# Kernel optimization log

Measured on AMD Instinct MI355X. Metric: run time of the kernel, lower is better.

Reference implementation:

```python
import jax, jax.numpy as jnp
import numpy as np

TEMPERATURE = 0.05
EPS = 1e-8  # torch.cosine_similarity eps


def setup_inputs() -> dict:
    key = jax.random.key(0)
    k1, k2 = jax.random.split(key)
    N, D = 8192, 256
    text_embeddings = jax.random.normal(k1, (N, D), dtype=jnp.float32)
    text_pos_embeddings = jax.random.normal(k2, (N, D), dtype=jnp.float32)
    return {"text_embeddings": text_embeddings, "text_pos_embeddings": text_pos_embeddings}


def reference(text_embeddings, text_pos_embeddings):
    # cosine similarity via normalize + single GEMM (same math as broadcasted
    # torch.cosine_similarity, which clamps norms at eps)
    a_norm = jnp.maximum(jnp.linalg.norm(text_embeddings, axis=-1, keepdims=True), EPS)
    b_norm = jnp.maximum(jnp.linalg.norm(text_pos_embeddings, axis=-1, keepdims=True), EPS)
    a = text_embeddings / a_norm  # [N, D]
    b = text_pos_embeddings / b_norm  # [N, D]
    sim = jnp.einsum("nd,md->nm", a, b) / TEMPERATURE  # [N, N]
    # cross-entropy with labels = arange(N): mean over rows of -log_softmax diag
    logp = jax.nn.log_softmax(sim, axis=-1)
    loss = -jnp.mean(jnp.diagonal(logp))
    return loss
```

## Files before the change

kernel.cpp:

```cpp
#include <hip/hip_runtime.h>
#include <math.h>

#define DIM 256

typedef float f32x4 __attribute__((ext_vector_type(4)));
typedef int   i32x8 __attribute__((ext_vector_type(8)));

__constant__ const float kTempInvLog2e = 20.0f * 1.4426950408889634f;
#define LN2 0.6931471805599453f
#define EPS_NORM 1e-8f
#define SCALE_ONE 0x7F7F7F7Fu

static __device__ inline unsigned f2fp8x4(float4 v, float s) {
    int r = 0;
    r = __builtin_amdgcn_cvt_pk_fp8_f32(v.x * s, v.y * s, r, false);
    r = __builtin_amdgcn_cvt_pk_fp8_f32(v.z * s, v.w * s, r, true);
    return (unsigned)r;
}

static __device__ inline i32x8 ld_frag32(const void* p0, const void* p1) {
    uint4 a = *(const uint4*)p0;
    uint4 b = *(const uint4*)p1;
    i32x8 v;
    v[0] = a.x; v[1] = a.y; v[2] = a.z; v[3] = a.w;
    v[4] = b.x; v[5] = b.y; v[6] = b.z; v[7] = b.w;
    return v;
}

__global__ __launch_bounds__(256) void normpack_kernel(
    const float* __restrict__ A, const float* __restrict__ B,
    unsigned char* __restrict__ Apk, unsigned char* __restrict__ Bpk,
    float* __restrict__ diag, float* __restrict__ rowsum, int n)
{
    __shared__ uint4 lA[256];
    __shared__ uint4 lB[256];
    const int t = threadIdx.x;
    const int rl = t >> 4;
    const int c16 = t & 15;
    const int r = blockIdx.x * 16 + rl;

    const float4* pa = (const float4*)(A + (size_t)r * DIM + c16 * 16);
    const float4* pb = (const float4*)(B + (size_t)r * DIM + c16 * 16);
    float4 a0 = pa[0], a1 = pa[1], a2 = pa[2], a3 = pa[3];
    float4 b0 = pb[0], b1 = pb[1], b2 = pb[2], b3 = pb[3];

    float ssa = a0.x*a0.x + a0.y*a0.y + a0.z*a0.z + a0.w*a0.w
              + a1.x*a1.x + a1.y*a1.y + a1.z*a1.z + a1.w*a1.w
              + a2.x*a2.x + a2.y*a2.y + a2.z*a2.z + a2.w*a2.w
              + a3.x*a3.x + a3.y*a3.y + a3.z*a3.z + a3.w*a3.w;
    float ssb = b0.x*b0.x + b0.y*b0.y + b0.z*b0.z + b0.w*b0.w
              + b1.x*b1.x + b1.y*b1.y + b1.z*b1.z + b1.w*b1.w
              + b2.x*b2.x + b2.y*b2.y + b2.z*b2.z + b2.w*b2.w
              + b3.x*b3.x + b3.y*b3.y + b3.z*b3.z + b3.w*b3.w;
    float dd  = a0.x*b0.x + a0.y*b0.y + a0.z*b0.z + a0.w*b0.w
              + a1.x*b1.x + a1.y*b1.y + a1.z*b1.z + a1.w*b1.w
              + a2.x*b2.x + a2.y*b2.y + a2.z*b2.z + a2.w*b2.w
              + a3.x*b3.x + a3.y*b3.y + a3.z*b3.z + a3.w*b3.w;
#pragma unroll
    for (int m = 1; m < 16; m <<= 1) {
        ssa += __shfl_xor(ssa, m, 64);
        ssb += __shfl_xor(ssb, m, 64);
        dd  += __shfl_xor(dd, m, 64);
    }
    float na = fmaxf(sqrtf(ssa), EPS_NORM);
    float nb = fmaxf(sqrtf(ssb), EPS_NORM);
    float sa = kTempInvLog2e / na;
    float sb = 1.0f / nb;
    if (c16 == 0) {
        diag[r] = dd / (na * nb) * kTempInvLog2e;
        rowsum[r] = 0.0f;
    }

    const int u = ((c16 >> 3) << 7) + ((c16 & 1) << 6) + rl + ((c16 & 7) >> 1) * 16;
    uint4 ga, gb;
    ga.x = f2fp8x4(a0, sa); ga.y = f2fp8x4(a1, sa);
    ga.z = f2fp8x4(a2, sa); ga.w = f2fp8x4(a3, sa);
    gb.x = f2fp8x4(b0, sb); gb.y = f2fp8x4(b1, sb);
    gb.z = f2fp8x4(b2, sb); gb.w = f2fp8x4(b3, sb);
    lA[u] = ga; lB[u] = gb;
    __syncthreads();

    ((uint4*)Apk)[(size_t)blockIdx.x * 256 + t] = lA[t];
    ((uint4*)Bpk)[(size_t)blockIdx.x * 256 + t] = lB[t];
}

static __device__ inline void async_copy16(const void* g, void* l) {
    __builtin_amdgcn_global_load_lds(
        (const __attribute__((address_space(1))) unsigned int*)g,
        (__attribute__((address_space(3))) unsigned int*)l, 16, 0, 0);
}

__global__ __launch_bounds__(256, 2) void gemm_lse_kernel(
    const unsigned char* __restrict__ Apk, const unsigned char* __restrict__ Bpk,
    float* __restrict__ rowsum, int n)
{
    __shared__ char ldsbuf[24576];
    const int lane = threadIdx.x & 63;
    const int w = threadIdx.x >> 6;
    const int c = lane & 15;
    const int q = lane >> 4;

    const int i = blockIdx.x;
    const int split = ((i & 7) << 1) | ((i >> 3) & 1);
    const int rowblk = i >> 4;
    const int rowbase = rowblk * 256 + w * 64;

    i32x8 afrag[4][2];
#pragma unroll
    for (int m = 0; m < 4; ++m) {
        const int AT = rowblk * 16 + w * 4 + m;
#pragma unroll
        for (int kc = 0; kc < 2; ++kc) {
            const char* base = (const char*)Apk + ((size_t)AT * 2 + kc) * 2048 + lane * 16;
            afrag[m][kc] = ld_frag32(base, base + 1024);
        }
    }

    float sums[16];
#pragma unroll
    for (int s = 0; s < 16; ++s) sums[s] = 0.0f;

    const char* bbase = (const char*)Bpk + (size_t)split * 32 * 4096;
    const int NITER = 16;

#pragma unroll
    for (int p = 0; p < 2; ++p) {
        const char* src = bbase + (size_t)p * 8192 + w * 2048 + (size_t)lane * 16;
        char* dst = ldsbuf + p * 8192 + w * 2048;
        async_copy16(src, dst);
        async_copy16(src + 1024, dst + 1024);
    }
    asm volatile("s_waitcnt vmcnt(2)" ::: "memory");
    __builtin_amdgcn_s_barrier();

#pragma unroll
    for (int it = 0; it < NITER; ++it) {
#pragma unroll
        for (int m = 0; m < 4; ++m)
#pragma unroll
            for (int kc = 0; kc < 2; ++kc)
                asm volatile("" : "+v"(afrag[m][kc]));

        const int cur = it % 3;
        const char* lb = ldsbuf + cur * 8192 + (size_t)lane * 16;

        i32x8 bfrag[2][2];
#pragma unroll
        for (int nc = 0; nc < 2; ++nc)
#pragma unroll
            for (int kc = 0; kc < 2; ++kc) {
                const char* p = lb + nc * 4096 + kc * 2048;
                bfrag[nc][kc] = ld_frag32(p, p + 1024);
            }

        if (it + 2 < NITER) {
            const int nb = (it + 2) % 3;
            const char* src = bbase + (size_t)(it + 2) * 8192 + w * 2048 + (size_t)lane * 16;
            char* dst = ldsbuf + nb * 8192 + w * 2048;
            async_copy16(src, dst);
            async_copy16(src + 1024, dst + 1024);
        }

        f32x4 acc[4][2];
#pragma unroll
        for (int m = 0; m < 4; ++m)
#pragma unroll
            for (int nc = 0; nc < 2; ++nc)
                acc[m][nc] = (f32x4){0.f, 0.f, 0.f, 0.f};

#pragma unroll
        for (int nc = 0; nc < 2; ++nc)
#pragma unroll
            for (int kc = 0; kc < 2; ++kc)
#pragma unroll
                for (int m = 0; m < 4; ++m)
                    acc[m][nc] = __builtin_amdgcn_mfma_scale_f32_16x16x128_f8f6f4(
                        afrag[m][kc], bfrag[nc][kc], acc[m][nc],
                        0, 0,
                        0, SCALE_ONE,
                        0, SCALE_ONE);

#pragma unroll
        for (int m = 0; m < 4; ++m)
#pragma unroll
            for (int nc = 0; nc < 2; ++nc)
#pragma unroll
                for (int r = 0; r < 4; ++r)
                    sums[m * 4 + r] += __builtin_amdgcn_exp2f(acc[m][nc][r]);

        if (it + 2 < NITER) {
            asm volatile("s_waitcnt vmcnt(2)" ::: "memory");
            __builtin_amdgcn_s_barrier();
        } else if (it + 1 < NITER) {
            asm volatile("s_waitcnt vmcnt(0)" ::: "memory");
            __builtin_amdgcn_s_barrier();
        }
    }

#pragma unroll
    for (int s = 0; s < 16; ++s) {
        float v = sums[s];
        v += __shfl_xor(v, 1, 64);
        v += __shfl_xor(v, 2, 64);
        v += __shfl_xor(v, 4, 64);
        v += __shfl_xor(v, 8, 64);
        sums[s] = v;
    }
    if (c == 0) {
#pragma unroll
        for (int m = 0; m < 4; ++m)
#pragma unroll
            for (int r = 0; r < 4; ++r)
                atomicAdd(&rowsum[rowbase + m * 16 + q * 4 + r], sums[m * 4 + r]);
    }
}

__global__ __launch_bounds__(1024) void finale_kernel(
    const float* __restrict__ rowsum, const float* __restrict__ diag,
    float* __restrict__ out, int n)
{
    __shared__ float red[1024];
    float local = 0.0f;
    for (int row = threadIdx.x; row < n; row += 1024)
        local += log2f(rowsum[row]) - diag[row];
    red[threadIdx.x] = local;
    __syncthreads();
    for (int off = 512; off > 0; off >>= 1) {
        if (threadIdx.x < off) red[threadIdx.x] += red[threadIdx.x + off];
        __syncthreads();
    }
    if (threadIdx.x == 0) out[0] = red[0] * (LN2 / (float)n);
}

extern "C" void kernel_launch(void* const* d_in, const int* in_sizes, int n_in,
                              void* d_out, int out_size, void* d_ws, size_t ws_size,
                              hipStream_t stream) {
    const int n = in_sizes[0] / DIM;
    const float* A = (const float*)d_in[0];
    const float* B = (const float*)d_in[1];
    float* out = (float*)d_out;

    unsigned char* Apk = (unsigned char*)d_ws;
    unsigned char* Bpk = Apk + (size_t)n * DIM;
    float* rowsum = (float*)(Bpk + (size_t)n * DIM);
    float* diag = rowsum + n;

    normpack_kernel<<<n / 16, 256, 0, stream>>>(A, B, Apk, Bpk, diag, rowsum, n);

    gemm_lse_kernel<<<(n / 256) * 16, 256, 0, stream>>>(Apk, Bpk, rowsum, n);

    finale_kernel<<<1, 1024, 0, stream>>>(rowsum, diag, out, n);
}
```

Baseline: 89.60 us.

## Replace triple-buffered B pipeline with two bulk 64KB LDS loads per block

The GEMM-LSE kernel drops its 3-stage rolling async LDS pipeline, which needed a barrier every iteration. It now loads half of the block's B slice (64KB) into LDS in one burst, waits for all of it, and computes 8 tiles with no barriers in between, then repeats for the second half. This cuts per-iteration synchronisation, but global loads no longer overlap compute inside a block. The 64KB of LDS per block also likely caps occupancy below the requested 2 blocks per CU, so any overlap has to come from other resident blocks.

```diff
diff --git a/kernel.cpp b/kernel.cpp
--- a/kernel.cpp
+++ b/kernel.cpp
@@ -94,7 +94,7 @@
     const unsigned char* __restrict__ Apk, const unsigned char* __restrict__ Bpk,
     float* __restrict__ rowsum, int n)
 {
-    __shared__ char ldsbuf[24576];
+    __shared__ char ldsbuf[65536];
     const int lane = threadIdx.x & 63;
     const int w = threadIdx.x >> 6;
     const int c = lane & 15;
@@ -120,81 +120,68 @@
 #pragma unroll
     for (int s = 0; s < 16; ++s) sums[s] = 0.0f;
 
-    const char* bbase = (const char*)Bpk + (size_t)split * 32 * 4096;
-    const int NITER = 16;
-
-#pragma unroll
-    for (int p = 0; p < 2; ++p) {
-        const char* src = bbase + (size_t)p * 8192 + w * 2048 + (size_t)lane * 16;
-        char* dst = ldsbuf + p * 8192 + w * 2048;
-        async_copy16(src, dst);
-        async_copy16(src + 1024, dst + 1024);
-    }
-    asm volatile("s_waitcnt vmcnt(2)" ::: "memory");
-    __builtin_amdgcn_s_barrier();
-
-#pragma unroll
-    for (int it = 0; it < NITER; ++it) {
-#pragma unroll
-        for (int m = 0; m < 4; ++m)
-#pragma unroll
-            for (int kc = 0; kc < 2; ++kc)
-                asm volatile("" : "+v"(afrag[m][kc]));
-
-        const int cur = it % 3;
-        const char* lb = ldsbuf + cur * 8192 + (size_t)lane * 16;
-
-        i32x8 bfrag[2][2];
-#pragma unroll
-        for (int nc = 0; nc < 2; ++nc)
-#pragma unroll
-            for (int kc = 0; kc < 2; ++kc) {
-                const char* p = lb + nc * 4096 + kc * 2048;
-                bfrag[nc][kc] = ld_frag32(p, p + 1024);
-            }
-
-        if (it + 2 < NITER) {
-            const int nb = (it + 2) % 3;
-            const char* src = bbase + (size_t)(it + 2) * 8192 + w * 2048 + (size_t)lane * 16;
-            char* dst = ldsbuf + nb * 8192 + w * 2048;
-            async_copy16(src, dst);
-            async_copy16(src + 1024, dst + 1024);
+    const char* bbase = (const char*)Bpk + (size_t)split * 131072;
+
+#pragma unroll 1
+    for (int h = 0; h < 2; ++h) {
+        {
+            const char* src = bbase + (size_t)h * 65536 + w * 16384 + (size_t)lane * 16;
+            char* dst = ldsbuf + w * 16384;
+#pragma unroll
+            for (int j = 0; j < 16; ++j)
+                async_copy16(src + j * 1024, dst + j * 1024);
         }
-
-        f32x4 acc[4][2];
-#pragma unroll
-        for (int m = 0; m < 4; ++m)
+        asm volatile("s_waitcnt vmcnt(0)" ::: "memory");
+        __builtin_amdgcn_s_barrier();
+
+#pragma unroll
+        for (int t8 = 0; t8 < 8; ++t8) {
+#pragma unroll
+            for (int m = 0; m < 4; ++m)
+#pragma unroll
+                for (int kc = 0; kc < 2; ++kc)
+                    asm volatile("" : "+v"(afrag[m][kc]));
+
+            const char* lb = ldsbuf + t8 * 8192 + (size_t)lane * 16;
+            i32x8 bfrag[2][2];
 #pragma unroll
             for (int nc = 0; nc < 2; ++nc)
-                acc[m][nc] = (f32x4){0.f, 0.f, 0.f, 0.f};
-
-#pragma unroll
-        for (int nc = 0; nc < 2; ++nc)
-#pragma unroll
-            for (int kc = 0; kc < 2; ++kc)
-#pragma unroll
-                for (int m = 0; m < 4; ++m)
-                    acc[m][nc] = __builtin_amdgcn_mfma_scale_f32_16x16x128_f8f6f4(
-                        afrag[m][kc], bfrag[nc][kc], acc[m][nc],
-                        0, 0,
-                        0, SCALE_ONE,
-                        0, SCALE_ONE);
-
-#pragma unroll
-        for (int m = 0; m < 4; ++m)
+#pragma unroll
+                for (int kc = 0; kc < 2; ++kc) {
+                    const char* p = lb + nc * 4096 + kc * 2048;
+                    bfrag[nc][kc] = ld_frag32(p, p + 1024);
+                }
+
+            f32x4 acc[4][2];
+#pragma unroll
+            for (int m = 0; m < 4; ++m)
+#pragma unroll
+                for (int nc = 0; nc < 2; ++nc)
+                    acc[m][nc] = (f32x4){0.f, 0.f, 0.f, 0.f};
+
 #pragma unroll
             for (int nc = 0; nc < 2; ++nc)
 #pragma unroll
-                for (int r = 0; r < 4; ++r)
-                    sums[m * 4 + r] += __builtin_amdgcn_exp2f(acc[m][nc][r]);
-
-        if (it + 2 < NITER) {
-            asm volatile("s_waitcnt vmcnt(2)" ::: "memory");
-            __builtin_amdgcn_s_barrier();
-        } else if (it + 1 < NITER) {
-            asm volatile("s_waitcnt vmcnt(0)" ::: "memory");
-            __builtin_amdgcn_s_barrier();
+                for (int kc = 0; kc < 2; ++kc)
+#pragma unroll
+                    for (int m = 0; m < 4; ++m)
+                        acc[m][nc] = __builtin_amdgcn_mfma_scale_f32_16x16x128_f8f6f4(
+                            afrag[m][kc], bfrag[nc][kc], acc[m][nc],
+                            0, 0,
+                            0, SCALE_ONE,
+                            0, SCALE_ONE);
+
+#pragma unroll
+            for (int m = 0; m < 4; ++m)
+#pragma unroll
+                for (int nc = 0; nc < 2; ++nc)
+#pragma unroll
+                    for (int r = 0; r < 4; ++r)
+                        sums[m * 4 + r] += __builtin_amdgcn_exp2f(acc[m][nc][r]);
         }
+
+        if (h == 0)
+            __syncthreads();
     }
 
 #pragma unroll
```

Result: slower. 94.32 us (+5.3%).
